# Optimization experiments

Hardware: AMD Instinct MI355X
Metric: run time of the kernel (lower is better)

Reference implementation:

```python
import jax, jax.numpy as jnp
import numpy as np

D_MODEL = 512

def setup_inputs() -> dict:
    key = jax.random.key(0)
    k1, k2, k3, k4, k5 = jax.random.split(key, 5)
    x = jax.random.normal(k1, (8, D_MODEL, 2048), dtype=jnp.float32)
    s = 1.0 / np.sqrt(D_MODEL)
    W_qkv = jax.random.uniform(k2, (D_MODEL, 3 * D_MODEL), dtype=jnp.float32, minval=-s, maxval=s)
    b_qkv = jax.random.uniform(k3, (3 * D_MODEL,), dtype=jnp.float32, minval=-s, maxval=s)
    W_proj = jax.random.uniform(k4, (D_MODEL, D_MODEL), dtype=jnp.float32, minval=-s, maxval=s)
    b_proj = jax.random.uniform(k5, (D_MODEL,), dtype=jnp.float32, minval=-s, maxval=s)
    return {"x": x, "W_qkv": W_qkv, "b_qkv": b_qkv, "W_proj": W_proj, "b_proj": b_proj}

def reference(x, W_qkv, b_qkv, W_proj, b_proj):
    # x: [B, L, N] with L == d_model; attend across the N variable axis
    xt = jnp.swapaxes(x, 1, 2)                      # [B, N, L]
    L = xt.shape[-1]
    qkv = xt @ W_qkv + b_qkv                        # [B, N, 3L]
    q, k, v = jnp.split(qkv, 3, axis=-1)            # each [B, N, L]
    attn = jnp.einsum('bnd,bmd->bnm', q, k) / jnp.sqrt(jnp.float32(L))
    attn = jax.nn.softmax(attn, axis=-1)            # [B, N, N]
    out = jnp.einsum('bnm,bmd->bnd', attn, v)       # [B, N, L]
    out = out @ W_proj + b_proj                     # [B, N, L]
    return jnp.swapaxes(out, 1, 2)                  # [B, L, N]
```

## Files before the change

kernel.cpp:

```cpp
#include <hip/hip_runtime.h>

#define NVAR 2048
#define DM   512
#define J3   1536

typedef _Float16 f16;
typedef _Float16 f16x8 __attribute__((ext_vector_type(8)));
typedef _Float16 f16x4 __attribute__((ext_vector_type(4)));
typedef float    f32x4 __attribute__((ext_vector_type(4)));

#define SBAR() do { asm volatile("s_barrier" ::: "memory"); \
                    __builtin_amdgcn_sched_barrier(0); } while(0)
#define LGKM0() do { asm volatile("s_waitcnt lgkmcnt(0)" ::: "memory"); \
                     __builtin_amdgcn_sched_barrier(0); } while(0)
#define GLOAD(gp, lp) __builtin_amdgcn_global_load_lds( \
    (const __attribute__((address_space(1))) void*)(gp), \
    (__attribute__((address_space(3))) void*)(lp), 16, 0, 0)

__device__ __forceinline__ void waitvm_n(int n) {
    switch (n) {
    case 0: asm volatile("s_waitcnt vmcnt(0)" ::: "memory"); break;
    case 1: asm volatile("s_waitcnt vmcnt(1)" ::: "memory"); break;
    case 2: asm volatile("s_waitcnt vmcnt(2)" ::: "memory"); break;
    case 3: asm volatile("s_waitcnt vmcnt(3)" ::: "memory"); break;
    case 4: asm volatile("s_waitcnt vmcnt(4)" ::: "memory"); break;
    case 5: asm volatile("s_waitcnt vmcnt(5)" ::: "memory"); break;
    case 6: asm volatile("s_waitcnt vmcnt(6)" ::: "memory"); break;
    case 7: asm volatile("s_waitcnt vmcnt(7)" ::: "memory"); break;
    case 8: asm volatile("s_waitcnt vmcnt(8)" ::: "memory"); break;
    default: break;
    }
    __builtin_amdgcn_sched_barrier(0);
}

__global__ __launch_bounds__(256)
void k_tr(const float* __restrict__ src, f16* __restrict__ dst,
          int R, int C, long bsSrc, long bsDst) {
    __shared__ float t[64][65];
    const float* s = src + (size_t)blockIdx.z * bsSrc;
    f16* d = dst + (size_t)blockIdx.z * bsDst;
    const int c0 = blockIdx.x * 64, r0 = blockIdx.y * 64;
    const int lx = threadIdx.x & 15, ly = threadIdx.x >> 4;
#pragma unroll
    for (int p = 0; p < 4; ++p) {
        int r = p * 16 + ly;
        f32x4 v = *(const f32x4*)(s + (size_t)(r0 + r) * C + c0 + lx * 4);
#pragma unroll
        for (int i = 0; i < 4; ++i) t[r][lx * 4 + i] = v[i];
    }
    __syncthreads();
#pragma unroll
    for (int p = 0; p < 4; ++p) {
        int c = p * 16 + ly;
        f16x4 h;
#pragma unroll
        for (int i = 0; i < 4; ++i) h[i] = (f16)t[lx * 4 + i][c];
        *(f16x4*)(d + (size_t)(c0 + c) * R + r0 + lx * 4) = h;
    }
}

#define ASZ (256 * 64)
__global__ __launch_bounds__(512, 2)
void gemm_sp(const f16* __restrict__ A, const f16* __restrict__ B,
             long bsA, long bsB, int lda, int ldb, int K,
             float scale, f16* __restrict__ o0) {
    __shared__ f16 smem[5 * ASZ];
    f16* sA = smem;
    f16* sB = smem + 3 * ASZ;

    const int tid  = threadIdx.x;
    const int lane = tid & 63;
    const int w    = __builtin_amdgcn_readfirstlane(tid >> 6);
    const int wm   = (w >> 2) * 128;
    const int wn   = (w & 3) * 64;
    const int z    = blockIdx.x;
    const int bid  = blockIdx.y;
    const int bxA  = bid & 7;
    const int bxB  = bid >> 3;

    const f16* Ab = A + (size_t)z * bsA + (size_t)bxA * 256 * lda;
    const f16* Bb = B + (size_t)z * bsB + (size_t)bxB * 256 * ldb;

    int offA[2][2], offB[2][2];
#pragma unroll
    for (int h = 0; h < 2; ++h)
#pragma unroll
        for (int i = 0; i < 2; ++i) {
            int slot = i * 512 + tid;
            int row  = h * 128 + (slot >> 3);
            int s    = (slot & 7) ^ (row & 7);
            offA[h][i] = row * lda + s * 8;
            offB[h][i] = row * ldb + s * 8;
        }

    auto STG_A = [&](int kt, int h, int buf) {
        f16* d = sA + buf * ASZ + h * 8192;
#pragma unroll
        for (int i = 0; i < 2; ++i)
            GLOAD(Ab + offA[h][i] + kt * 64, d + (i * 512 + tid) * 8);
    };
    auto STG_B = [&](int kt, int h, int buf) {
        f16* d = sB + buf * ASZ + h * 8192;
#pragma unroll
        for (int i = 0; i < 2; ++i)
            GLOAD(Bb + offB[h][i] + kt * 64, d + (i * 512 + tid) * 8);
    };

    int koff[2];
#pragma unroll
    for (int ks = 0; ks < 2; ++ks)
        koff[ks] = ((ks * 4 + (lane >> 4)) ^ (lane & 7)) * 8;
    const int rowA = (wm + (lane & 15)) * 64;
    const int rowB = (wn + (lane & 15)) * 64;

    f16x8 av[8][2], bv[4][2];
    f32x4 acc[8][4] = {};

    auto LD_AV = [&](const f16* p, int mi0) {
#pragma unroll
        for (int mi = 0; mi < 4; ++mi)
#pragma unroll
            for (int ks = 0; ks < 2; ++ks)
                av[mi0 + mi][ks] = *(const f16x8*)(p + rowA + (mi0 + mi) * 1024 + koff[ks]);
    };
    auto LD_BV = [&](const f16* p, int nj0) {
#pragma unroll
        for (int nj = 0; nj < 2; ++nj)
#pragma unroll
            for (int ks = 0; ks < 2; ++ks)
                bv[nj0 + nj][ks] = *(const f16x8*)(p + rowB + (nj0 + nj) * 1024 + koff[ks]);
    };
    auto MM = [&](int mi0, int nj0) {
        __builtin_amdgcn_s_setprio(1);
#pragma unroll
        for (int mi = 0; mi < 4; ++mi)
#pragma unroll
            for (int nj = 0; nj < 2; ++nj)
#pragma unroll
                for (int ks = 0; ks < 2; ++ks)
                    acc[mi0 + mi][nj0 + nj] = __builtin_amdgcn_mfma_f32_16x16x32_f16(
                        av[mi0 + mi][ks], bv[nj0 + nj][ks], acc[mi0 + mi][nj0 + nj], 0, 0, 0);
        __builtin_amdgcn_s_setprio(0);
    };

    const int NT = K >> 6;
    int issued = 0, markB = 0;

    STG_A(0, 0, 0); STG_A(0, 1, 0); issued += 4;
    STG_B(0, 0, 0); STG_B(0, 1, 0); issued += 4; markB = issued;
    if (NT > 1) { STG_A(1, 0, 1); STG_A(1, 1, 1); issued += 4; }
    waitvm_n(issued - markB);
    SBAR();

    int iA = 0, iB = 0;
    for (int t = 0; t < NT; ++t) {
        const f16* pA = sA + iA * ASZ;
        const f16* pB = sB + iB * ASZ;
        const int bufB2 = iB ^ 1;
        int bufA2 = iA + 2; if (bufA2 >= 3) bufA2 -= 3;

        LD_BV(pB, 0); LD_AV(pA, 0);
        if (t + 1 < NT) { STG_B(t + 1, 0, bufB2); issued += 2; }
        SBAR(); LGKM0();
        MM(0, 0);
        SBAR();
        LD_BV(pB, 2);
        if (t + 1 < NT) { STG_B(t + 1, 1, bufB2); issued += 2; markB = issued; }
        SBAR(); LGKM0();
        MM(0, 2);
        SBAR();
        LD_AV(pA, 4);
        if (t + 2 < NT) { STG_A(t + 2, 0, bufA2); issued += 2; }
        SBAR(); LGKM0();
        MM(4, 2);
        SBAR();
        if (t + 2 < NT) { STG_A(t + 2, 1, bufA2); issued += 2; }
        if (t + 1 < NT) { waitvm_n(issued - markB); SBAR(); }
        MM(4, 0);
        if (t + 1 < NT) SBAR();

        iA = (iA + 1 == 3) ? 0 : iA + 1;
        iB ^= 1;
    }

    const int rb0 = bxA * 256 + wm + (lane >> 4) * 4;
    const int cb0 = bxB * 256 + wn + (lane & 15);
#pragma unroll
    for (int mi = 0; mi < 8; ++mi)
#pragma unroll
        for (int nj = 0; nj < 4; ++nj) {
            f16x4 vv;
#pragma unroll
            for (int r = 0; r < 4; ++r)
                vv[r] = (f16)__expf(acc[mi][nj][r] * scale);
            *(f16x4*)(o0 + ((size_t)z * NVAR + cb0 + nj * 16) * NVAR
                           + rb0 + mi * 16) = vv;
        }
}

template<int MODE>
__global__ __launch_bounds__(256)
void gemm_f16(const f16* __restrict__ A, const f16* __restrict__ B,
              long bsA, long bsB, int lda, int ldb, int K, int nbx,
              const float* __restrict__ bias,
              f16* __restrict__ o0, f16* __restrict__ o1, f16* __restrict__ o2,
              float* __restrict__ of) {
    __shared__ f16 sA[128 * 64];
    __shared__ f16 sB[128 * 64];
    const int tid  = threadIdx.x;
    const int lane = tid & 63;
    const int w    = __builtin_amdgcn_readfirstlane(tid >> 6);
    const int wm   = (w >> 1) * 64;
    const int wn   = (w & 1) * 64;
    const int z    = blockIdx.x;
    const int bid  = blockIdx.y;
    const int bxA  = bid % nbx;
    const int bxB  = bid / nbx;

    const f16* Ab = A + (size_t)z * bsA + (size_t)bxA * 128 * lda;
    const f16* Bb = B + (size_t)z * bsB + (size_t)bxB * 128 * ldb;

    int srcA[4], srcB[4];
#pragma unroll
    for (int i = 0; i < 4; ++i) {
        int slot = i * 256 + tid;
        int row  = slot >> 3;
        int s    = (slot & 7) ^ (row & 7);
        srcA[i] = row * lda + s * 8;
        srcB[i] = row * ldb + s * 8;
    }

    f16x8 ones;
#pragma unroll
    for (int e = 0; e < 8; ++e) ones[e] = (f16)1.0f;

    f32x4 acc[4][4] = {};
    f32x4 accrs[4] = {};

    for (int k0 = 0; k0 < K; k0 += 64) {
        __syncthreads();
#pragma unroll
        for (int i = 0; i < 4; ++i) {
            GLOAD(Ab + srcA[i] + k0, sA + i * 2048 + w * 512);
            GLOAD(Bb + srcB[i] + k0, sB + i * 2048 + w * 512);
        }
        __syncthreads();
#pragma unroll
        for (int kh = 0; kh < 2; ++kh) {
            f16x8 av[4], bv[4];
#pragma unroll
            for (int mi = 0; mi < 4; ++mi) {
                int r = wm + mi * 16 + (lane & 15);
                int s = (kh * 4 + (lane >> 4)) ^ (r & 7);
                av[mi] = *(const f16x8*)(sA + r * 64 + s * 8);
            }
#pragma unroll
            for (int nj = 0; nj < 4; ++nj) {
                int r = wn + nj * 16 + (lane & 15);
                int s = (kh * 4 + (lane >> 4)) ^ (r & 7);
                bv[nj] = *(const f16x8*)(sB + r * 64 + s * 8);
            }
            if constexpr (MODE == 2) {
#pragma unroll
                for (int nj = 0; nj < 4; ++nj)
                    accrs[nj] = __builtin_amdgcn_mfma_f32_16x16x32_f16(
                        ones, bv[nj], accrs[nj], 0, 0, 0);
            }
#pragma unroll
            for (int mi = 0; mi < 4; ++mi)
#pragma unroll
                for (int nj = 0; nj < 4; ++nj)
                    acc[mi][nj] = __builtin_amdgcn_mfma_f32_16x16x32_f16(
                        av[mi], bv[nj], acc[mi][nj], 0, 0, 0);
        }
    }

    const int rb0 = bxA * 128 + wm + (lane >> 4) * 4;
    const int cb0 = bxB * 128 + wn + (lane & 15);

    if (MODE == 0) {
        const int seg = (bxA * 128) >> 9;
#pragma unroll
        for (int mi = 0; mi < 4; ++mi) {
            const int j = rb0 + mi * 16;
            const f32x4 b4 = *(const f32x4*)(bias + j);
#pragma unroll
            for (int nj = 0; nj < 4; ++nj) {
                const int n = cb0 + nj * 16;
                if (seg == 2) {
#pragma unroll
                    for (int r = 0; r < 4; ++r)
                        o2[((size_t)z * DM + (j - 1024 + r)) * NVAR + n] =
                            (f16)(acc[mi][nj][r] + b4[r]);
                } else {
                    f16* dst = seg ? o1 : o0;
                    const int jj = seg ? j - 512 : j;
                    f16x4 vv;
#pragma unroll
                    for (int r = 0; r < 4; ++r) vv[r] = (f16)(acc[mi][nj][r] + b4[r]);
                    *(f16x4*)(dst + ((size_t)z * NVAR + n) * DM + jj) = vv;
                }
            }
        }
    } else if (MODE == 2) {
        float inv[4];
#pragma unroll
        for (int nj = 0; nj < 4; ++nj) inv[nj] = 1.0f / accrs[nj][0];
#pragma unroll
        for (int mi = 0; mi < 4; ++mi)
#pragma unroll
            for (int nj = 0; nj < 4; ++nj) {
                f16x4 vv;
#pragma unroll
                for (int r = 0; r < 4; ++r)
                    vv[r] = (f16)(acc[mi][nj][r] * inv[nj]);
                *(f16x4*)(o0 + ((size_t)z * NVAR + cb0 + nj * 16) * DM
                               + rb0 + mi * 16) = vv;
            }
    } else {
#pragma unroll
        for (int mi = 0; mi < 4; ++mi)
#pragma unroll
            for (int nj = 0; nj < 4; ++nj) {
                const int l = cb0 + nj * 16;
                const float bb = bias[l];
                f32x4 vv;
#pragma unroll
                for (int r = 0; r < 4; ++r) vv[r] = acc[mi][nj][r] + bb;
                *(f32x4*)(of + ((size_t)z * DM + l) * NVAR + rb0 + mi * 16) = vv;
            }
    }
}

extern "C" void kernel_launch(void* const* d_in, const int* in_sizes, int n_in,
                              void* d_out, int out_size, void* d_ws, size_t ws_size,
                              hipStream_t stream) {
    const float* x     = (const float*)d_in[0];
    const float* Wqkv  = (const float*)d_in[1];
    const float* bqkv  = (const float*)d_in[2];
    const float* Wproj = (const float*)d_in[3];
    const float* bproj = (const float*)d_in[4];
    float* out = (float*)d_out;

    const size_t PB = (size_t)NVAR * DM;
    f16* xT  = (f16*)d_ws;
    f16* q   = xT + 8 * PB;
    f16* kk  = q  + 8 * PB;
    f16* vT  = kk + 8 * PB;
    f16* S   = vT + 8 * PB;
    f16* O   = S  + (size_t)8 * NVAR * NVAR;
    f16* WqT = O  + 8 * PB;
    f16* WpT = WqT + (size_t)J3 * DM;

    k_tr<<<dim3(NVAR / 64, DM / 64, 8), 256, 0, stream>>>(
        x, xT, DM, NVAR, (long)DM * NVAR, (long)NVAR * DM);
    k_tr<<<dim3(J3 / 64, DM / 64, 1), 256, 0, stream>>>(Wqkv, WqT, DM, J3, 0, 0);
    k_tr<<<dim3(DM / 64, DM / 64, 1), 256, 0, stream>>>(Wproj, WpT, DM, DM, 0, 0);

    gemm_f16<0><<<dim3(8, 12 * 16), 256, 0, stream>>>(
        WqT, xT, 0, (long)NVAR * DM, DM, DM, DM, 12,
        bqkv, q, kk, vT, nullptr);

    gemm_sp<<<dim3(8, 8 * 8), 512, 0, stream>>>(
        kk, q, (long)NVAR * DM, (long)NVAR * DM, DM, DM, DM,
        0.044194173824159216f, S);

    gemm_f16<2><<<dim3(8, 4 * 16), 256, 0, stream>>>(
        vT, S, (long)DM * NVAR, (long)NVAR * NVAR, NVAR, NVAR, NVAR, 4,
        nullptr, O, nullptr, nullptr, nullptr);

    gemm_f16<3><<<dim3(8, 16 * 4), 256, 0, stream>>>(
        O, WpT, (long)NVAR * DM, 0, DM, DM, DM, 16,
        bproj, nullptr, nullptr, nullptr, out);
}
```

Baseline: 180.4 us.

## Fold output projection into V weights and fuse PV with final projection

Precomputes W_v·W_proj (and the folded bias b_v·W_proj) so the V projection directly produces V·W_proj. The attention-times-V GEMM then yields the final output with softmax normalisation and bias applied in its epilogue. This removes the separate output projection GEMM and the intermediate O buffer. A new 512-thread kernel with triple-buffered A tiles and 256x128 block tiles replaces the old PV GEMM. The weight product is rounded to f16 before use, which adds some precision risk, and a small weight-prep GEMM plus two tiny kernels are added per call.

```diff
diff --git a/kernel.cpp b/kernel.cpp
--- a/kernel.cpp
+++ b/kernel.cpp
@@ -59,6 +59,33 @@
     }
 }
 
+__global__ __launch_bounds__(256)
+void k_cast(const float* __restrict__ W, f16* __restrict__ out) {
+    int idx = blockIdx.x * 256 + threadIdx.x;
+    int gi = idx * 4;
+    int d = gi >> 9, j = gi & 511;
+    f32x4 v = *(const f32x4*)(W + (size_t)d * J3 + 1024 + j);
+    f16x4 h;
+#pragma unroll
+    for (int i = 0; i < 4; ++i) h[i] = (f16)v[i];
+    *(f16x4*)(out + (size_t)d * 512 + j) = h;
+}
+
+__global__ __launch_bounds__(512)
+void k_bvp(const float* __restrict__ bqkv, const float* __restrict__ Wp,
+           float* __restrict__ bias_c) {
+    const int l = threadIdx.x;
+    float a[8] = {};
+    for (int j = 0; j < 512; j += 8)
+#pragma unroll
+        for (int u = 0; u < 8; ++u)
+            a[u] += bqkv[1024 + j + u] * Wp[(size_t)(j + u) * DM + l];
+    float s = ((a[0] + a[1]) + (a[2] + a[3])) + ((a[4] + a[5]) + (a[6] + a[7]));
+    bias_c[1024 + l] = s;
+    bias_c[l] = bqkv[l];
+    bias_c[512 + l] = bqkv[512 + l];
+}
+
 #define ASZ (256 * 64)
 __global__ __launch_bounds__(512, 2)
 void gemm_sp(const f16* __restrict__ A, const f16* __restrict__ B,
@@ -164,16 +191,19 @@
         SBAR(); LGKM0();
         MM(0, 0);
         SBAR();
+
         LD_BV(pB, 2);
         if (t + 1 < NT) { STG_B(t + 1, 1, bufB2); issued += 2; markB = issued; }
         SBAR(); LGKM0();
         MM(0, 2);
         SBAR();
+
         LD_AV(pA, 4);
         if (t + 2 < NT) { STG_A(t + 2, 0, bufA2); issued += 2; }
         SBAR(); LGKM0();
         MM(4, 2);
         SBAR();
+
         if (t + 2 < NT) { STG_A(t + 2, 1, bufA2); issued += 2; }
         if (t + 1 < NT) { waitvm_n(issued - markB); SBAR(); }
         MM(4, 0);
@@ -196,6 +226,155 @@
             *(f16x4*)(o0 + ((size_t)z * NVAR + cb0 + nj * 16) * NVAR
                            + rb0 + mi * 16) = vv;
         }
+}
+
+#define BSZO (128 * 64)
+__global__ __launch_bounds__(512, 2)
+void gemm_out(const f16* __restrict__ A, const f16* __restrict__ B,
+              long bsA, long bsB, int lda, int ldb, int K,
+              const float* __restrict__ bias, float* __restrict__ of) {
+    __shared__ f16 smem[3 * ASZ + 2 * BSZO];
+    f16* sA = smem;
+    f16* sB = smem + 3 * ASZ;
+
+    const int tid  = threadIdx.x;
+    const int lane = tid & 63;
+    const int w    = __builtin_amdgcn_readfirstlane(tid >> 6);
+    const int wm   = (w >> 1) * 64;
+    const int wn   = (w & 1) * 64;
+    const int z    = blockIdx.x;
+    const int bid  = blockIdx.y;
+    const int bxA  = bid & 7;
+    const int bxB  = bid >> 3;
+
+    const f16* Ab = A + (size_t)z * bsA + (size_t)bxA * 256 * lda;
+    const f16* Bb = B + (size_t)z * bsB + (size_t)bxB * 128 * ldb;
+
+    int offA[2][2], offB[2];
+#pragma unroll
+    for (int h = 0; h < 2; ++h)
+#pragma unroll
+        for (int i = 0; i < 2; ++i) {
+            int slot = i * 512 + tid;
+            int row  = h * 128 + (slot >> 3);
+            int s    = (slot & 7) ^ (row & 7);
+            offA[h][i] = row * lda + s * 8;
+        }
+#pragma unroll
+    for (int h = 0; h < 2; ++h) {
+        int row = h * 64 + (tid >> 3);
+        int s   = (tid & 7) ^ (row & 7);
+        offB[h] = row * ldb + s * 8;
+    }
+
+    auto STG_A = [&](int kt, int buf) {
+        f16* d = sA + buf * ASZ;
+#pragma unroll
+        for (int h = 0; h < 2; ++h)
+#pragma unroll
+            for (int i = 0; i < 2; ++i)
+                GLOAD(Ab + offA[h][i] + kt * 64, d + h * 8192 + (i * 512 + tid) * 8);
+    };
+    auto STG_B = [&](int kt, int buf) {
+        f16* d = sB + buf * BSZO;
+#pragma unroll
+        for (int h = 0; h < 2; ++h)
+            GLOAD(Bb + offB[h] + kt * 64, d + h * 4096 + tid * 8);
+    };
+
+    int koff[2];
+#pragma unroll
+    for (int ks = 0; ks < 2; ++ks)
+        koff[ks] = ((ks * 4 + (lane >> 4)) ^ (lane & 7)) * 8;
+    const int rowA = (wm + (lane & 15)) * 64;
+    const int rowB = (wn + (lane & 15)) * 64;
+
+    f16x8 ones;
+#pragma unroll
+    for (int e = 0; e < 8; ++e) ones[e] = (f16)1.0f;
+
+    f16x8 av[4][2], bv[4][2];
+    f32x4 acc[4][4] = {};
+    f32x4 accrs[4] = {};
+
+    auto LD_AV = [&](const f16* p, int mi0) {
+#pragma unroll
+        for (int mi = 0; mi < 2; ++mi)
+#pragma unroll
+            for (int ks = 0; ks < 2; ++ks)
+                av[mi0 + mi][ks] = *(const f16x8*)(p + rowA + (mi0 + mi) * 1024 + koff[ks]);
+    };
+    auto LD_BV = [&](const f16* p) {
+#pragma unroll
+        for (int nj = 0; nj < 4; ++nj)
+#pragma unroll
+            for (int ks = 0; ks < 2; ++ks)
+                bv[nj][ks] = *(const f16x8*)(p + rowB + nj * 1024 + koff[ks]);
+    };
+    auto MM = [&](int mi0) {
+        __builtin_amdgcn_s_setprio(1);
+#pragma unroll
+        for (int mi = 0; mi < 2; ++mi)
+#pragma unroll
+            for (int ks = 0; ks < 2; ++ks) {
+                accrs[mi0 + mi] = __builtin_amdgcn_mfma_f32_16x16x32_f16(
+                    av[mi0 + mi][ks], ones, accrs[mi0 + mi], 0, 0, 0);
+#pragma unroll
+                for (int nj = 0; nj < 4; ++nj)
+                    acc[mi0 + mi][nj] = __builtin_amdgcn_mfma_f32_16x16x32_f16(
+                        av[mi0 + mi][ks], bv[nj][ks], acc[mi0 + mi][nj], 0, 0, 0);
+            }
+        __builtin_amdgcn_s_setprio(0);
+    };
+
+    const int NT = K >> 6;
+    int issued = 0, markB = 0;
+
+    STG_A(0, 0); issued += 4;
+    STG_B(0, 0); issued += 2; markB = issued;
+    if (NT > 1) { STG_A(1, 1); issued += 4; }
+    waitvm_n(issued - markB);
+    SBAR();
+
+    int iA = 0, iB = 0;
+    for (int t = 0; t < NT; ++t) {
+        const f16* pA = sA + iA * ASZ;
+        const f16* pB = sB + iB * BSZO;
+        int bufA2 = iA + 2; if (bufA2 >= 3) bufA2 -= 3;
+
+        LD_BV(pB); LD_AV(pA, 0);
+        if (t + 1 < NT) { STG_B(t + 1, iB ^ 1); issued += 2; markB = issued; }
+        SBAR(); LGKM0();
+        MM(0);
+        SBAR();
+
+        LD_AV(pA, 2);
+        if (t + 2 < NT) { STG_A(t + 2, bufA2); issued += 4; }
+        SBAR(); LGKM0();
+        MM(2);
+        if (t + 1 < NT) { waitvm_n(issued - markB); SBAR(); }
+
+        iA = (iA + 1 == 3) ? 0 : iA + 1;
+        iB ^= 1;
+    }
+
+    const int rb0 = bxA * 256 + wm + (lane >> 4) * 4;
+    const int cb0 = bxB * 128 + wn + (lane & 15);
+#pragma unroll
+    for (int mi = 0; mi < 4; ++mi) {
+        f32x4 inv;
+#pragma unroll
+        for (int r = 0; r < 4; ++r) inv[r] = 1.0f / accrs[mi][r];
+#pragma unroll
+        for (int nj = 0; nj < 4; ++nj) {
+            const int l = cb0 + nj * 16;
+            const float bb = bias[l];
+            f32x4 vv;
+#pragma unroll
+            for (int r = 0; r < 4; ++r) vv[r] = acc[mi][nj][r] * inv[r] + bb;
+            *(f32x4*)(of + ((size_t)z * DM + l) * NVAR + rb0 + mi * 16) = vv;
+        }
+    }
 }
 
 template<int MODE>
@@ -203,8 +382,7 @@
 void gemm_f16(const f16* __restrict__ A, const f16* __restrict__ B,
               long bsA, long bsB, int lda, int ldb, int K, int nbx,
               const float* __restrict__ bias,
-              f16* __restrict__ o0, f16* __restrict__ o1, f16* __restrict__ o2,
-              float* __restrict__ of) {
+              f16* __restrict__ o0, f16* __restrict__ o1, f16* __restrict__ o2) {
     __shared__ f16 sA[128 * 64];
     __shared__ f16 sB[128 * 64];
     const int tid  = threadIdx.x;
@@ -230,12 +408,7 @@
         srcB[i] = row * ldb + s * 8;
     }
 
-    f16x8 ones;
-#pragma unroll
-    for (int e = 0; e < 8; ++e) ones[e] = (f16)1.0f;
-
     f32x4 acc[4][4] = {};
-    f32x4 accrs[4] = {};
 
     for (int k0 = 0; k0 < K; k0 += 64) {
         __syncthreads();
@@ -259,12 +432,6 @@
                 int r = wn + nj * 16 + (lane & 15);
                 int s = (kh * 4 + (lane >> 4)) ^ (r & 7);
                 bv[nj] = *(const f16x8*)(sB + r * 64 + s * 8);
-            }
-            if constexpr (MODE == 2) {
-#pragma unroll
-                for (int nj = 0; nj < 4; ++nj)
-                    accrs[nj] = __builtin_amdgcn_mfma_f32_16x16x32_f16(
-                        ones, bv[nj], accrs[nj], 0, 0, 0);
             }
 #pragma unroll
             for (int mi = 0; mi < 4; ++mi)
@@ -302,32 +469,16 @@
                 }
             }
         }
-    } else if (MODE == 2) {
-        float inv[4];
-#pragma unroll
-        for (int nj = 0; nj < 4; ++nj) inv[nj] = 1.0f / accrs[nj][0];
+    } else {
 #pragma unroll
         for (int mi = 0; mi < 4; ++mi)
 #pragma unroll
             for (int nj = 0; nj < 4; ++nj) {
                 f16x4 vv;
 #pragma unroll
-                for (int r = 0; r < 4; ++r)
-                    vv[r] = (f16)(acc[mi][nj][r] * inv[nj]);
-                *(f16x4*)(o0 + ((size_t)z * NVAR + cb0 + nj * 16) * DM
+                for (int r = 0; r < 4; ++r) vv[r] = (f16)acc[mi][nj][r];
+                *(f16x4*)(o0 + ((size_t)(cb0 + nj * 16)) * DM
                                + rb0 + mi * 16) = vv;
-            }
-    } else {
-#pragma unroll
-        for (int mi = 0; mi < 4; ++mi)
-#pragma unroll
-            for (int nj = 0; nj < 4; ++nj) {
-                const int l = cb0 + nj * 16;
-                const float bb = bias[l];
-                f32x4 vv;
-#pragma unroll
-                for (int r = 0; r < 4; ++r) vv[r] = acc[mi][nj][r] + bb;
-                *(f32x4*)(of + ((size_t)z * DM + l) * NVAR + rb0 + mi * 16) = vv;
             }
     }
 }
@@ -343,33 +494,37 @@
     float* out = (float*)d_out;
 
     const size_t PB = (size_t)NVAR * DM;
-    f16* xT  = (f16*)d_ws;
-    f16* q   = xT + 8 * PB;
-    f16* kk  = q  + 8 * PB;
-    f16* vT  = kk + 8 * PB;
-    f16* S   = vT + 8 * PB;
-    f16* O   = S  + (size_t)8 * NVAR * NVAR;
-    f16* WqT = O  + 8 * PB;
-    f16* WpT = WqT + (size_t)J3 * DM;
+    f16* xT   = (f16*)d_ws;
+    f16* q    = xT + 8 * PB;
+    f16* kk   = q  + 8 * PB;
+    f16* vwT  = kk + 8 * PB;
+    f16* S    = vwT + 8 * PB;
+    f16* scr  = S  + (size_t)8 * NVAR * NVAR;
+    f16* WqT  = scr + 8 * PB;
+    f16* WpT  = WqT + (size_t)J3 * DM;
+    f16* Wq2  = scr;
+    float* bias_c = (float*)(scr + 512 * 512);
 
     k_tr<<<dim3(NVAR / 64, DM / 64, 8), 256, 0, stream>>>(
         x, xT, DM, NVAR, (long)DM * NVAR, (long)NVAR * DM);
-    k_tr<<<dim3(J3 / 64, DM / 64, 1), 256, 0, stream>>>(Wqkv, WqT, DM, J3, 0, 0);
+    k_tr<<<dim3(16, DM / 64, 1), 256, 0, stream>>>(Wqkv, WqT, DM, J3, 0, 0);
     k_tr<<<dim3(DM / 64, DM / 64, 1), 256, 0, stream>>>(Wproj, WpT, DM, DM, 0, 0);
+    k_cast<<<dim3(256), 256, 0, stream>>>(Wqkv, Wq2);
+    k_bvp<<<dim3(1), 512, 0, stream>>>(bqkv, Wproj, bias_c);
+
+    gemm_f16<4><<<dim3(1, 16), 256, 0, stream>>>(
+        Wq2, WpT, 0, 0, 512, DM, DM, 4,
+        nullptr, WqT + (size_t)1024 * DM, nullptr, nullptr);
 
     gemm_f16<0><<<dim3(8, 12 * 16), 256, 0, stream>>>(
         WqT, xT, 0, (long)NVAR * DM, DM, DM, DM, 12,
-        bqkv, q, kk, vT, nullptr);
+        bias_c, q, kk, vwT);
 
     gemm_sp<<<dim3(8, 8 * 8), 512, 0, stream>>>(
         kk, q, (long)NVAR * DM, (long)NVAR * DM, DM, DM, DM,
         0.044194173824159216f, S);
 
-    gemm_f16<2><<<dim3(8, 4 * 16), 256, 0, stream>>>(
-        vT, S, (long)DM * NVAR, (long)NVAR * NVAR, NVAR, NVAR, NVAR, 4,
-        nullptr, O, nullptr, nullptr, nullptr);
-
-    gemm_f16<3><<<dim3(8, 16 * 4), 256, 0, stream>>>(
-        O, WpT, (long)NVAR * DM, 0, DM, DM, DM, 16,
-        bproj, nullptr, nullptr, nullptr, out);
-}
+    gemm_out<<<dim3(8, 32), 512, 0, stream>>>(
+        S, vwT, (long)NVAR * NVAR, (long)DM * NVAR, NVAR, NVAR, NVAR,
+        bproj, out);
+}
```

New measurement: 187.6 us. 4.0% more time.
